# Kernel optimization log

Measured on AMD Instinct MI355X. Metric: run time of the kernel, lower is better.

The kernel has to match this reference:

```python
import jax, jax.numpy as jnp
import numpy as np

MU_F, SIGMA_F, ALPHA = 0.0789, 0.0774, 1.0
THRESH = MU_F + ALPHA * SIGMA_F
B, H, W = 8, 768, 768


def _gabor_kernel_real(frequency, theta):
    # skimage.filters.gabor_kernel with bandwidth=1, n_stds=3; real part only
    sigma = (1.0 / np.pi * np.sqrt(np.log(2.0) / 2.0) * 3.0) / frequency  # ~5.622
    ct, st = np.cos(theta), np.sin(theta)
    x0 = int(np.ceil(max(abs(3 * sigma * ct), abs(3 * sigma * st), 1.0)))
    y0 = int(np.ceil(max(abs(3 * sigma * st), abs(3 * sigma * ct), 1.0)))
    y, x = np.mgrid[-y0:y0 + 1, -x0:x0 + 1]
    rotx = x * ct + y * st
    roty = -x * st + y * ct
    g = np.exp(-0.5 * (rotx ** 2 + roty ** 2) / sigma ** 2) / (2 * np.pi * sigma ** 2)
    return (g * np.cos(2 * np.pi * frequency * rotx)).astype(np.float32)


# pre-flip 180deg so cross-correlation == scipy.ndimage.convolve (true convolution)
GABOR = [jnp.asarray(np.ascontiguousarray(_gabor_kernel_real(0.1, np.radians(a))[::-1, ::-1]))
         for a in (45, 90, 135, 180)]

_SIG = 0.3 * ((101 - 1) * 0.5 - 1) + 0.8  # cv2 sigma for ksize=101 when sigma=0 -> 15.5
_xg = np.arange(101, dtype=np.float64) - 50.0
_g = np.exp(-_xg ** 2 / (2 * _SIG ** 2))
GAUSS = jnp.asarray((_g / _g.sum()).astype(np.float32))
SOBEL_X = jnp.asarray(np.array([[-1, 0, 1], [-2, 0, 2], [-1, 0, 1]], np.float32))
SOBEL_Y = SOBEL_X.T


def _corr2d(img, k, mode):
    # 'same' cross-correlation with chosen boundary mode
    kh, kw = k.shape
    p = jnp.pad(img, ((kh // 2, kh // 2), (kw // 2, kw // 2)), mode=mode)
    return jax.lax.conv_general_dilated(p[None, None], k[None, None], (1, 1), 'VALID')[0, 0]


def _maxfilt3(img):
    # scipy.ndimage.maximum_filter(size=3, mode='reflect') == jnp 'symmetric' pad
    p = jnp.pad(img, 1, mode='symmetric')
    return jax.lax.reduce_window(p, -jnp.inf, jax.lax.max, (3, 3), (1, 1), 'VALID')


def _flood(maskf, seedf):
    # region growing == union of 8-connected components of {grad>=T} containing a seed;
    # iterate masked 3x3 dilation to fixed point
    reach0 = maskf * seedf

    def body(s):
        r, _ = s
        dil = jax.lax.reduce_window(jnp.pad(r, 1), 0.0, jax.lax.max, (3, 3), (1, 1), 'VALID')
        new = jnp.maximum(r, dil * maskf)
        return new, jnp.any(new != r)

    r, _ = jax.lax.while_loop(lambda s: s[1], body, (reach0, jnp.array(True)))
    return r


def _forward_one(pred, img):
    img = (img - img.min()) / (img.max() - img.min())
    # cv2.GaussianBlur((101,101), 0) with BORDER_REFLECT_101 -> 'reflect', separable
    bg = _corr2d(_corr2d(img, GAUSS[None, :], 'reflect'), GAUSS[:, None], 'reflect')
    enh = jnp.clip(img - bg, 0.0, 1.0)
    # seed points: Gabor line detection at 4 angles, local maxima above mean
    seed = jnp.zeros(enh.shape, bool)
    for k in GABOR:
        f = _corr2d(enh, k, 'symmetric')  # ndimage.convolve mode='reflect'
        seed = seed | ((f == _maxfilt3(f)) & (f > f.mean()))
    # Sobel gradient magnitude (cv2 default BORDER_REFLECT_101 -> 'reflect')
    gx = _corr2d(enh, SOBEL_X, 'reflect')
    gy = _corr2d(enh, SOBEL_Y, 'reflect')
    grad = jnp.sqrt(gx ** 2 + gy ** 2)
    maskf = (grad >= THRESH).astype(jnp.float32)
    seg = jax.lax.stop_gradient(_flood(maskf, seed.astype(jnp.float32)))
    # sigmoid only if prediction is outside [0,1]
    need_sig = (pred.max() > 1.0) | (pred.min() < 0.0)
    p = jnp.where(need_sig, jax.nn.sigmoid(pred), pred)
    return ((p > 0.5) | (seg > 0)).astype(jnp.float32)


def setup_inputs() -> dict:
    key = jax.random.key(0)
    k1, k2 = jax.random.split(key)
    unet_output = jax.random.normal(k1, (B, 1, H, W), jnp.float32) * 2.0  # logits
    original_image = jax.random.uniform(k2, (B, 1, H, W), jnp.float32)
    return {"unet_output": unet_output, "original_image": original_image}


def reference(unet_output, original_image):
    out = jax.vmap(_forward_one)(unet_output[:, 0], original_image[:, 0])
    return out[:, None]  # [B,1,H,W]
```

## Files before the change

kernel.cpp:

```cpp
#include <hip/hip_runtime.h>
#include <math.h>

typedef unsigned long long u64;

#define W 768
#define H 768
#define NP (768*768)
#define NB 8
#define WPR 12
#define NW (NB*H*WPR)
#define TH 16
#define P12N 73728
#define FLOOD_PASSES 6

#define PADI(q) ((q) + ((q) >> 5))


__device__ __forceinline__ unsigned fenc(float f) {
    unsigned b = __float_as_uint(f);
    return b ^ ((unsigned)((int)b >> 31) | 0x80000000u);
}
__device__ __forceinline__ float fdec(unsigned u) {
    unsigned b = (u & 0x80000000u) ? (u ^ 0x80000000u) : ~u;
    return __uint_as_float(b);
}
__device__ __forceinline__ int refl101(int i, int n) {
    if (i < 0) i = -i;
    if (i >= n) i = 2*n - 2 - i;
    return i;
}
__device__ __forceinline__ int symref(int i, int n) {
    if (i < 0) i = -1 - i;
    if (i >= n) i = 2*n - 1 - i;
    return i;
}

__global__ void initK(float* wtab, unsigned* sc) {
    int t = threadIdx.x;
    double sig = 15.5, ssum = 0.0;
    for (int i = 0; i < 101; i++) { double xx = i - 50; ssum += exp(-xx*xx/(2.0*sig*sig)); }
    for (int i = t; i < 107; i += 256) {
        float v = 0.f; int j = i - 3;
        if (j >= 0 && j < 101) { double xx = j - 50; v = (float)(exp(-xx*xx/(2.0*sig*sig))/ssum); }
        wtab[i] = v;
    }
    for (int i = t; i < 163; i += 256) {
        float v = 0.f; int j = i - 31;
        if (j >= 0 && j < 101) { double xx = j - 50; v = (float)(exp(-xx*xx/(2.0*sig*sig))/ssum); }
        wtab[128 + i] = v;
    }
    const double thetas[4] = {45.0, 90.0, 135.0, 180.0};
    const int    rad[4]    = {12, 17, 12, 17};
    const double sg = ((1.0/M_PI) * sqrt(log(2.0)/2.0) * 3.0) / 0.1;
    const double C  = 1.0/(2.0*M_PI*sg*sg);
    const int hG[6]   = {0, 0, 1, 2, 2, 3};
    const int hSin[6] = {0, 1, 0, 0, 1, 0};
    for (int idx = t; idx < 6*64; idx += 256) {
        int p = idx / 64, i = idx % 64;
        int g = hG[p], r = rad[g];
        double th = thetas[g] * (M_PI / 180.0);
        double a  = 2.0*M_PI*0.1*cos(th);
        float v = 0.f;
        int d = i - 20;
        if (i < 41 && d >= -r && d <= r) {
            double dd = (double)d, G = exp(-0.5*dd*dd/(sg*sg));
            v = hSin[p] ? (float)(C*G*sin(a*dd)) : (float)(C*G*cos(a*dd));
        }
        wtab[384 + p*64 + i] = v;
    }
    const int vG[6]   = {0, 0, 1, 2, 2, 3};
    const int vSin[6] = {0, 1, 0, 0, 1, 0};
    for (int idx = t; idx < 6*128; idx += 256) {
        int q = idx / 128, i = idx % 128;
        int g = vG[q], r = rad[g];
        double th = thetas[g] * (M_PI / 180.0);
        double bb = 2.0*M_PI*0.1*sin(th);
        float v = 0.f;
        int j = i - 31;
        if (j >= 0 && j <= 2*r) {
            double dd = (double)(j - r), G = exp(-0.5*dd*dd/(sg*sg));
            v = vSin[q] ? (float)(G*sin(bb*dd)) : (float)(G*cos(bb*dd));
        }
        wtab[768 + q*128 + i] = v;
    }
    if (t < 8)  { sc[t] = 0xFFFFFFFFu; sc[8+t] = 0u; sc[16+t] = 0xFFFFFFFFu; sc[24+t] = 0u; }
    if (t >= 32 && t < 64) ((float*)sc)[t] = 0.f;
    if (t >= 64 && t < 128) sc[t] = 0u;
}

__global__ void reduceK(const float* __restrict__ img, const float* __restrict__ pred,
                        unsigned* sc) {
    int b = blockIdx.y;
    int base = b*NP + blockIdx.x*9216 + threadIdx.x;
    float imn = INFINITY, imx = -INFINITY, pmn = INFINITY, pmx = -INFINITY;
    for (int k = 0; k < 36; k++) {
        float v = img[base + k*256];  imn = fminf(imn, v); imx = fmaxf(imx, v);
        float p = pred[base + k*256]; pmn = fminf(pmn, p); pmx = fmaxf(pmx, p);
    }
    for (int off = 32; off; off >>= 1) {
        imn = fminf(imn, __shfl_down(imn, off));
        imx = fmaxf(imx, __shfl_down(imx, off));
        pmn = fminf(pmn, __shfl_down(pmn, off));
        pmx = fmaxf(pmx, __shfl_down(pmx, off));
    }
    __shared__ float s[4][4];
    int lane = threadIdx.x & 63, wv = threadIdx.x >> 6;
    if (lane == 0) { s[0][wv] = imn; s[1][wv] = imx; s[2][wv] = pmn; s[3][wv] = pmx; }
    __syncthreads();
    if (threadIdx.x == 0) {
        float a0 = s[0][0], a1 = s[1][0], a2 = s[2][0], a3 = s[3][0];
        for (int w = 1; w < 4; w++) {
            a0 = fminf(a0, s[0][w]); a1 = fmaxf(a1, s[1][w]);
            a2 = fminf(a2, s[2][w]); a3 = fmaxf(a3, s[3][w]);
        }
        atomicMin(&sc[b],      fenc(a0));
        atomicMax(&sc[8 + b],  fenc(a1));
        atomicMin(&sc[16 + b], fenc(a2));
        atomicMax(&sc[24 + b], fenc(a3));
    }
}

__global__ __launch_bounds__(192) void gaussHK2(const float* __restrict__ img,
                                                float* __restrict__ out,
                                                const float* __restrict__ wt,
                                                const unsigned* __restrict__ sc) {
    int b = blockIdx.y, y = blockIdx.x, t = threadIdx.x;
    float mn = fdec(sc[b]), mx = fdec(sc[8 + b]);
    float den = mx - mn;
    __shared__ float sh[896];
    const float* row = img + ((size_t)b*H + y)*W;
    for (int q = t; q < 868; q += 192) {
        int gx = refl101(q - 50, W);
        sh[PADI(q)] = (row[gx] - mn) / den;
    }
    __syncthreads();
    float a0 = 0.f, a1 = 0.f, a2 = 0.f, a3 = 0.f;
    int qb = 4*t;
    #pragma unroll
    for (int p = 0; p < 104; p++) {
        float v = sh[PADI(qb + p)];
        a0 = __fmaf_rn(wt[p + 3], v, a0);
        a1 = __fmaf_rn(wt[p + 2], v, a1);
        a2 = __fmaf_rn(wt[p + 1], v, a2);
        a3 = __fmaf_rn(wt[p    ], v, a3);
    }
    float4 o; o.x = a0; o.y = a1; o.z = a2; o.w = a3;
    *(float4*)(out + ((size_t)b*H + y)*W + qb) = o;
}

__global__ __launch_bounds__(128) void gaussVK4(const float* __restrict__ tmp,
                                                const float* __restrict__ img,
                                                float* __restrict__ enh,
                                                const float* __restrict__ wt,
                                                const unsigned* __restrict__ sc) {
    int bid = blockIdx.x;
    int b = bid & 7; int r_ = bid >> 3; int tile = r_ % 48; int strip = r_ / 48;
    int y0 = tile*TH, x = strip*128 + threadIdx.x;
    float acc[TH];
    #pragma unroll
    for (int k = 0; k < TH; k++) acc[k] = 0.f;
    const float* T = tmp + (size_t)b*NP;
    for (int base = 0; base < 116; base += 4) {
        int g0 = refl101(y0+base-50, H), g1 = refl101(y0+base-49, H),
            g2 = refl101(y0+base-48, H), g3 = refl101(y0+base-47, H);
        float v0 = T[g0*W+x], v1 = T[g1*W+x], v2 = T[g2*W+x], v3 = T[g3*W+x];
        #pragma unroll
        for (int k = 0; k < TH; k++) {
            float a = acc[k];
            a = __fmaf_rn(wt[base   -k+31], v0, a);
            a = __fmaf_rn(wt[base+1 -k+31], v1, a);
            a = __fmaf_rn(wt[base+2 -k+31], v2, a);
            a = __fmaf_rn(wt[base+3 -k+31], v3, a);
            acc[k] = a;
        }
    }
    float mn = fdec(sc[b]), mx = fdec(sc[8 + b]);
    float den = mx - mn;
    #pragma unroll
    for (int k = 0; k < TH; k++) {
        size_t o = ((size_t)b*H + y0 + k)*W + x;
        float vv = (img[o] - mn) / den;
        float e = vv - acc[k];
        e = fminf(fmaxf(e, 0.f), 1.f);
        enh[o] = e;
    }
}

__global__ __launch_bounds__(192) void gaborHF4(const float* __restrict__ enh,
        float* __restrict__ h0c, float* __restrict__ h0s,
        float* __restrict__ h1c, float* __restrict__ h3c,
        const float* __restrict__ wt) {
    int b = blockIdx.y, y = blockIdx.x, t = threadIdx.x;
    __shared__ float sh[832];
    const float* row = enh + ((size_t)b*H + y)*W;
    for (int q = t; q < 802; q += 192) {
        int gx = symref(q - 17, W);
        sh[PADI(q)] = row[gx];
    }
    __syncthreads();
    const float* T0c = wt + 384; const float* T0s = wt + 448;
    const float* T1c = wt + 512; const float* T3c = wt + 704;
    float a0c[4] = {0,0,0,0}, a0s[4] = {0,0,0,0};
    float a1c[4] = {0,0,0,0}, a3c[4] = {0,0,0,0};
    int qb = 4*t;
    #pragma unroll
    for (int p = 0; p < 38; p++) {
        float v = sh[PADI(qb + p)];
        #pragma unroll
        for (int sub = 0; sub < 4; sub++) {
            int idx = p + 3 - sub;
            a0c[sub] = __fmaf_rn(T0c[idx], v, a0c[sub]);
            a0s[sub] = __fmaf_rn(T0s[idx], v, a0s[sub]);
            a1c[sub] = __fmaf_rn(T1c[idx], v, a1c[sub]);
            a3c[sub] = __fmaf_rn(T3c[idx], v, a3c[sub]);
        }
    }
    size_t o = ((size_t)b*H + y)*W + qb;
    *(float4*)(h0c + o) = make_float4(a0c[0], a0c[1], a0c[2], a0c[3]);
    *(float4*)(h0s + o) = make_float4(a0s[0], a0s[1], a0s[2], a0s[3]);
    *(float4*)(h1c + o) = make_float4(a1c[0], a1c[1], a1c[2], a1c[3]);
    *(float4*)(h3c + o) = make_float4(a3c[0], a3c[1], a3c[2], a3c[3]);
}

__global__ __launch_bounds__(128) void gaborVAB(
        const float* __restrict__ hc, const float* __restrict__ hs,
        float* __restrict__ f0, float* __restrict__ f2,
        const float* __restrict__ Tc, const float* __restrict__ Ts,
        float* __restrict__ p0, float* __restrict__ p2) {
    int bid = blockIdx.x;
    int b = bid & 7; int r_ = bid >> 3; int tile = r_ % 48; int strip = r_ / 48;
    int y0 = tile*TH, x = strip*128 + threadIdx.x;
    float A[TH], Bm[TH];
    #pragma unroll
    for (int k = 0; k < TH; k++) { A[k] = 0.f; Bm[k] = 0.f; }
    const size_t pb = (size_t)b*NP;
    for (int base = 0; base < 50; base += 2) {
        int gA = symref(y0 + base - 17, H), gB = symref(y0 + base - 16, H);
        size_t oA = pb + (size_t)gA*W + x, oB = pb + (size_t)gB*W + x;
        float vcA = hc[oA], vsA = hs[oA];
        float vcB = hc[oB], vsB = hs[oB];
        #pragma unroll
        for (int k = 0; k < TH; k++) {
            int i26 = base - k + 26;
            float t = A[k];
            t = __fmaf_rn(Tc[i26],   vcA, t);
            t = __fmaf_rn(Tc[i26+1], vcB, t);
            A[k] = t;
            t = Bm[k];
            t = __fmaf_rn(Ts[i26],   vsA, t);
            t = __fmaf_rn(Ts[i26+1], vsB, t);
            Bm[k] = t;
        }
    }
    int g64 = strip*2 + (threadIdx.x >> 6);
    bool l0 = (threadIdx.x & 63) == 0;
    #pragma unroll
    for (int k = 0; k < TH; k++) {
        size_t o = ((size_t)b*H + y0 + k)*W + x;
        size_t po = ((size_t)b*H + y0 + k)*12 + g64;
        float v0 = A[k] - Bm[k];
        float v2 = A[k] + Bm[k];
        f0[o] = v0;
        float s = v0;
        for (int off = 32; off; off >>= 1) s += __shfl_down(s, off);
        if (l0) p0[po] = s;
        f2[o] = v2;
        s = v2;
        for (int off = 32; off; off >>= 1) s += __shfl_down(s, off);
        if (l0) p2[po] = s;
    }
}

__global__ __launch_bounds__(128) void gaborV13(
        const float* __restrict__ h1, const float* __restrict__ h3,
        float* __restrict__ f1, float* __restrict__ f3,
        const float* __restrict__ T1, const float* __restrict__ T3,
        float* __restrict__ p1, float* __restrict__ p3) {
    int bid = blockIdx.x;
    int b = bid & 7; int r_ = bid >> 3; int tile = r_ % 48; int strip = r_ / 48;
    int y0 = tile*TH, x = strip*128 + threadIdx.x;
    float a1[TH], a3[TH];
    #pragma unroll
    for (int k = 0; k < TH; k++) { a1[k] = 0.f; a3[k] = 0.f; }
    const size_t pb = (size_t)b*NP;
    for (int base = 0; base < 50; base += 2) {
        int gA = symref(y0 + base - 17, H), gB = symref(y0 + base - 16, H);
        size_t oA = pb + (size_t)gA*W + x, oB = pb + (size_t)gB*W + x;
        float v1A = h1[oA], v3A = h3[oA];
        float v1B = h1[oB], v3B = h3[oB];
        #pragma unroll
        for (int k = 0; k < TH; k++) {
            int i31 = base - k + 31;
            float t = a1[k];
            t = __fmaf_rn(T1[i31],   v1A, t);
            t = __fmaf_rn(T1[i31+1], v1B, t);
            a1[k] = t;
            t = a3[k];
            t = __fmaf_rn(T3[i31],   v3A, t);
            t = __fmaf_rn(T3[i31+1], v3B, t);
            a3[k] = t;
        }
    }
    int g64 = strip*2 + (threadIdx.x >> 6);
    bool l0 = (threadIdx.x & 63) == 0;
    #pragma unroll
    for (int k = 0; k < TH; k++) {
        size_t o = ((size_t)b*H + y0 + k)*W + x;
        size_t po = ((size_t)b*H + y0 + k)*12 + g64;
        f1[o] = a1[k];
        float s = a1[k];
        for (int off = 32; off; off >>= 1) s += __shfl_down(s, off);
        if (l0) p1[po] = s;
        f3[o] = a3[k];
        s = a3[k];
        for (int off = 32; off; off >>= 1) s += __shfl_down(s, off);
        if (l0) p3[po] = s;
    }
}

__global__ void sumKAll(const float* __restrict__ p12, float* fsum) {
    int b = blockIdx.x, g = blockIdx.y, t = threadIdx.x;
    const float* P = p12 + (size_t)g*P12N;
    float s = 0.f;
    for (int k = 0; k < 9; k++) {
        int idx = t + k*256;
        int row = idx / 3, strip = idx - row*3;
        const float* Q = P + ((size_t)b*H + row)*12 + strip*4;
        float p4 = ((Q[0] + Q[1]) + Q[2]) + Q[3];
        s += p4;
    }
    __shared__ float sm[256];
    sm[t] = s; __syncthreads();
    for (int off = 128; off; off >>= 1) {
        if (t < off) sm[t] += sm[t + off];
        __syncthreads();
    }
    if (t == 0) fsum[g*8 + b] = sm[0];
}

__global__ __launch_bounds__(256) void seedK4(const float* __restrict__ f0,
        const float* __restrict__ f1, const float* __restrict__ f2,
        const float* __restrict__ f3, const float* __restrict__ fsum,
        u64* __restrict__ seedB) {
    int bid = blockIdx.x;
    int b = bid & 7; int r_ = bid >> 3;
    int y0 = (r_ % 48)*16; int xb = r_ / 48;
    int x0 = xb*256, t = threadIdx.x;
    __shared__ float sh[18][258];
    const float* planes[4] = {f0, f1, f2, f3};
    unsigned condMask = 0;
    #pragma unroll
    for (int a = 0; a < 4; a++) {
        const float* F = planes[a] + (size_t)b*NP;
        __syncthreads();
        for (int idx = t; idx < 18*258; idx += 256) {
            int rr = idx / 258, q = idx - rr*258;
            int gy = y0 - 1 + rr; gy = gy < 0 ? 0 : (gy > H-1 ? H-1 : gy);
            int gx = x0 - 1 + q;  gx = gx < 0 ? 0 : (gx > W-1 ? W-1 : gx);
            sh[rr][q] = F[gy*W + gx];
        }
        __syncthreads();
        float mean = fsum[a*8 + b] / 589824.f;
        #pragma unroll
        for (int r = 0; r < 16; r++) {
            float c = sh[r+1][t+1];
            float mx = c;
            mx = fmaxf(mx, sh[r  ][t]); mx = fmaxf(mx, sh[r  ][t+1]); mx = fmaxf(mx, sh[r  ][t+2]);
            mx = fmaxf(mx, sh[r+1][t]); mx = fmaxf(mx, sh[r+1][t+1]); mx = fmaxf(mx, sh[r+1][t+2]);
            mx = fmaxf(mx, sh[r+2][t]); mx = fmaxf(mx, sh[r+2][t+1]); mx = fmaxf(mx, sh[r+2][t+2]);
            if ((c == mx) && (c > mean)) condMask |= (1u << r);
        }
    }
    int wv = t >> 6, lane = t & 63;
    #pragma unroll
    for (int r = 0; r < 16; r++) {
        u64 m = __ballot((condMask >> r) & 1u);
        if (lane == 0)
            seedB[((size_t)b*H + y0 + r)*WPR + xb*4 + wv] = m;
    }
}

__global__ void sobelK(const float* __restrict__ enh, u64* __restrict__ maskB) {
    int bid = blockIdx.x;
    int b = bid & 7; int r_ = bid >> 3;
    int y = r_ / 3; int xs = r_ - 3*y;
    int x = xs*256 + threadIdx.x;
    const float* E = enh + (size_t)b*NP;
    int ym = y > 0 ? y-1 : 1, yp = y < H-1 ? y+1 : H-2;
    int xm = x > 0 ? x-1 : 1, xp = x < W-1 ? x+1 : W-2;
    float a00 = E[ym*W + xm], a01 = E[ym*W + x], a02 = E[ym*W + xp];
    float a10 = E[y*W + xm],                     a12 = E[y*W + xp];
    float a20 = E[yp*W + xm], a21 = E[yp*W + x], a22 = E[yp*W + xp];
    float gx = __fmaf_rn(-1.f, a00, 0.f);
    gx = __fmaf_rn( 1.f, a02, gx);
    gx = __fmaf_rn(-2.f, a10, gx);
    gx = __fmaf_rn( 2.f, a12, gx);
    gx = __fmaf_rn(-1.f, a20, gx);
    gx = __fmaf_rn( 1.f, a22, gx);
    float gy = __fmaf_rn(-1.f, a00, 0.f);
    gy = __fmaf_rn(-2.f, a01, gy);
    gy = __fmaf_rn(-1.f, a02, gy);
    gy = __fmaf_rn( 1.f, a20, gy);
    gy = __fmaf_rn( 2.f, a21, gy);
    gy = __fmaf_rn( 1.f, a22, gy);
    float s = __fadd_rn(__fmul_rn(gx, gx), __fmul_rn(gy, gy));
    float grad = (float)sqrt((double)s);
    const float THR = (float)(0.0789 + 1.0*0.0774);
    bool m = grad >= THR;
    u64 bits = __ballot(m);
    if ((threadIdx.x & 63) == 0) {
        int word = xs*4 + (threadIdx.x >> 6);
        maskB[((size_t)b*H + y)*WPR + word] = bits;
    }
}

__global__ __launch_bounds__(256) void floodTileK(const u64* __restrict__ Mb,
        const u64* __restrict__ seedB, u64* __restrict__ Rb,
        unsigned* __restrict__ chg, int t) {
    if (t > 0 && chg[t-1] == 0) return;
    int b = blockIdx.y;
    int y0 = blockIdx.x * 256;
    int ty = threadIdx.x;
    int y = y0 + ty;
    const u64* M = Mb + (size_t)b*H*WPR;
    const u64* S = seedB + (size_t)b*H*WPR;
    u64* R = Rb + (size_t)b*H*WPR;
    u64 m[12], r[12], hT[12], hB[12];
    #pragma unroll
    for (int w = 0; w < 12; w++) {
        m[w] = M[y*WPR + w];
        r[w] = (t == 0) ? (m[w] & S[y*WPR + w]) : R[y*WPR + w];
    }
    bool topRow = (ty == 0), botRow = (ty == 255);
    #pragma unroll
    for (int w = 0; w < 12; w++) { hT[w] = 0ULL; hB[w] = 0ULL; }
    if (topRow && y0 > 0) {
        int hy = y0 - 1;
        #pragma unroll
        for (int w = 0; w < 12; w++)
            hT[w] = (t == 0) ? (M[hy*WPR+w] & S[hy*WPR+w]) : R[hy*WPR+w];
    }
    if (botRow && y0 + 256 < H) {
        int hy = y0 + 256;
        #pragma unroll
        for (int w = 0; w < 12; w++)
            hB[w] = (t == 0) ? (M[hy*WPR+w] & S[hy*WPR+w]) : R[hy*WPR+w];
    }
    __shared__ u64 L[256][12];
    __shared__ unsigned chgArr[4];
    #pragma unroll
    for (int w = 0; w < 12; w++) L[ty][w] = r[w];
    __syncthreads();
    int wvid = ty >> 6, lane = ty & 63;
    bool grew = false;
    while (true) {
        u64 D[12], F[12];
        #pragma unroll
        for (int w = 0; w < 12; w++) {
            u64 up = topRow ? hT[w] : L[ty-1][w];
            u64 dn = botRow ? hB[w] : L[ty+1][w];
            D[w] = r[w] | up | dn;
        }
        #pragma unroll
        for (int w = 0; w < 12; w++) {
            u64 s = D[w] | (D[w] << 1) | (D[w] >> 1);
            if (w > 0)  s |= D[w-1] >> 63;
            if (w < 11) s |= D[w+1] << 63;
            F[w] = s & m[w];
        }
        {
            u64 c = 0;
            #pragma unroll
            for (int w = 0; w < 12; w++) {
                u64 sd = (F[w] | c) & m[w];
                u64 uf = m[w] & ~(m[w] + sd);
                F[w] = uf | sd;
                c = uf >> 63;
            }
        }
        {
            u64 c = 0;
            #pragma unroll
            for (int w = 11; w >= 0; w--) {
                u64 sd = (F[w] | (c << 63)) & m[w];
                u64 bm = __brevll(m[w]);
                u64 df = __brevll(bm & ~(bm + __brevll(sd)));
                F[w] = df | sd;
                c = df & 1ULL;
            }
        }
        bool chgT = false;
        #pragma unroll
        for (int w = 0; w < 12; w++) if (F[w] != r[w]) chgT = true;
        bool wc = __any(chgT);
        if (lane == 0) chgArr[wvid] = wc ? 1u : 0u;
        __syncthreads();
        #pragma unroll
        for (int w = 0; w < 12; w++) { r[w] = F[w]; L[ty][w] = F[w]; }
        unsigned any = chgArr[0] | chgArr[1] | chgArr[2] | chgArr[3];
        __syncthreads();
        if (!any) break;
        grew = true;
    }
    #pragma unroll
    for (int w = 0; w < 12; w++) R[y*WPR + w] = r[w];
    if (grew && ty == 0) atomicOr(&chg[t], 1u);
}

__global__ void finalK(const float* __restrict__ pred, const u64* __restrict__ reachB,
                       const unsigned* __restrict__ sc, float* __restrict__ out) {
    int b = blockIdx.z, y = blockIdx.y, x = blockIdx.x*256 + threadIdx.x;
    float pmn = fdec(sc[16 + b]), pmx = fdec(sc[24 + b]);
    bool needSig = (pmx > 1.0f) || (pmn < 0.0f);
    float p = pred[((size_t)b*H + y)*W + x];
    float pv;
    if (needSig) {
        float e = (float)exp(-(double)p);
        pv = 1.f / (1.f + e);
    } else {
        pv = p;
    }
    bool on = pv > 0.5f;
    u64 w = reachB[((size_t)b*H + y)*WPR + (x >> 6)];
    on = on || ((w >> (x & 63)) & 1ULL);
    out[((size_t)b*H + y)*W + x] = on ? 1.f : 0.f;
}

extern "C" void kernel_launch(void* const* d_in, const int* in_sizes, int n_in,
                              void* d_out, int out_size, void* d_ws, size_t ws_size,
                              hipStream_t stream) {
    const float* pred = (const float*)d_in[0];
    const float* img  = (const float*)d_in[1];
    float* out = (float*)d_out;
    char* ws = (char*)d_ws;

    float*    wtab   = (float*)(ws + 1024);
    unsigned* sc     = (unsigned*)(ws + 16384);
    float*    fsum   = ((float*)sc) + 32;
    unsigned* chg    = sc + 64;
    float*    p12    = (float*)(ws + 20480);
    u64*      maskB  = (u64*)(ws + 1310720);
    u64*      seedB  = (u64*)(ws + 1900544);
    u64*      reachB = (u64*)(ws + 2490368);
    const size_t PL = (size_t)NB*NP;
    float* plane = (float*)(ws + 4194304);
    float* b0  = plane;
    float* b1  = plane + PL;
    float* h0c = plane + 2*PL; float* h0s = plane + 3*PL;
    float* h1c = plane + 4*PL; float* h3c = plane + 5*PL;
    float* f0  = plane + 8*PL; float* f1 = plane + 9*PL;
    float* f2  = plane + 10*PL; float* f3 = plane + 11*PL;

    const float* gpadH = wtab;
    const float* gpadV = wtab + 128;

    initK<<<1, 256, 0, stream>>>(wtab, sc);
    reduceK<<<dim3(64, 8), 256, 0, stream>>>(img, pred, sc);

    dim3 gRow(768, 8);
    gaussHK2<<<gRow, 192, 0, stream>>>(img, b0, gpadH, sc);
    gaussVK4<<<2304, 128, 0, stream>>>(b0, img, b1, gpadV, sc);

    sobelK<<<18432, 256, 0, stream>>>(b1, maskB);

    gaborHF4<<<gRow, 192, 0, stream>>>(b1, h0c, h0s, h1c, h3c, wtab);

    gaborVAB<<<2304, 128, 0, stream>>>(h0c, h0s, f0, f2,
                                       wtab + 768, wtab + 896,
                                       p12, p12 + 2*P12N);
    gaborV13<<<2304, 128, 0, stream>>>(h1c, h3c, f1, f3,
                                       wtab + 1024, wtab + 1408,
                                       p12 + P12N, p12 + 3*P12N);
    sumKAll<<<dim3(8, 4), 256, 0, stream>>>(p12, fsum);

    seedK4<<<1152, 256, 0, stream>>>(f0, f1, f2, f3, fsum, seedB);

    for (int t = 0; t < FLOOD_PASSES; t++)
        floodTileK<<<dim3(3, 8), 256, 0, stream>>>(maskB, seedB, reachB, chg, t);

    finalK<<<dim3(3, H, 8), 256, 0, stream>>>(pred, reachB, sc, out);
}
```

Measured before the change: 254.8 us.

## Fuse seed detection into vertical Gabor passes and compute filter means analytically

The vertical Gabor kernels now compute the 3x3 local-max seed test in registers, using shuffles and shared memory for neighbours, and write seed bitmasks directly. This removes the four full-resolution filter-response planes and the separate seed kernel. Tile-boundary columns are spilled to a small buffer and finished by a tiny edge kernel. Each filter's global mean is now computed from row sums of the enhanced image using precomputed boundary-aware weight tables, instead of reducing the responses. The cost is recomputing two halo rows per tile and added code complexity.

```diff
diff --git a/kernel.cpp b/kernel.cpp
--- a/kernel.cpp
+++ b/kernel.cpp
@@ -10,7 +10,6 @@
 #define WPR 12
 #define NW (NB*H*WPR)
 #define TH 16
-#define P12N 73728
 #define FLOOD_PASSES 6
 
 #define PADI(q) ((q) + ((q) >> 5))
@@ -34,8 +33,11 @@
     if (i >= n) i = 2*n - 1 - i;
     return i;
 }
-
-__global__ void initK(float* wtab, unsigned* sc) {
+__device__ __forceinline__ size_t fbIdx(int g, int b, int strip, int c4, int row) {
+    return ((((size_t)g*NB + b)*6 + strip)*4 + c4)*768 + row;
+}
+
+__global__ void initK(float* wtab, float* cwv, unsigned* sc) {
     int t = threadIdx.x;
     double sig = 15.5, ssum = 0.0;
     for (int i = 0; i < 101; i++) { double xx = i - 50; ssum += exp(-xx*xx/(2.0*sig*sig)); }
@@ -86,6 +88,42 @@
     if (t < 8)  { sc[t] = 0xFFFFFFFFu; sc[8+t] = 0u; sc[16+t] = 0xFFFFFFFFu; sc[24+t] = 0u; }
     if (t >= 32 && t < 64) ((float*)sc)[t] = 0.f;
     if (t >= 64 && t < 128) sc[t] = 0u;
+    __syncthreads();
+    const int hTab[4] = {0, 1, 2, 5};
+    const int vTab[4] = {0, 1, 2, 5};
+    const int Rv[4]   = {12, 12, 17, 17};
+    if (t < 4) {
+        const float* T = wtab + 384 + hTab[t]*64;
+        float s = 0.f;
+        for (int i = 0; i < 41; i++) s += T[i];
+        wtab[1808 + t] = s;
+    }
+    for (int idx = t; idx < 4*68; idx += 256) {
+        int ch = idx / 68, e = idx % 68;
+        int c = (e < 34) ? e : 734 + (e - 34);
+        const float* T = wtab + 384 + hTab[ch]*64;
+        float w = 0.f;
+        int lo = c - 767; if (lo < -20) lo = -20;
+        int hi = c;       if (hi > 20)  hi = 20;
+        for (int d = lo; d <= hi; d++) w += T[d + 20];
+        if (c <= 19)  { for (int d = -20; d <= -1 - c; d++) w += T[d + 20]; }
+        if (c >= 748) { for (int d = 768 - c; d <= 20; d++) w += T[d + 20]; }
+        float s = 0.f;
+        for (int i = 0; i < 41; i++) s += T[i];
+        wtab[1536 + ch*68 + e] = w - s;
+    }
+    for (int idx = t; idx < 4*768; idx += 256) {
+        int ch = idx / 768, r = idx % 768;
+        const float* V = wtab + 768 + vTab[ch]*128;
+        int off = 31 + Rv[ch];
+        float w = 0.f;
+        int lo = r - 767; if (lo < -17) lo = -17;
+        int hi = r;       if (hi > 17)  hi = 17;
+        for (int e = lo; e <= hi; e++) w += V[off + e];
+        if (r <= 16)  { for (int e = -17; e <= -1 - r; e++) w += V[off + e]; }
+        if (r >= 751) { for (int e = 768 - r; e <= 17; e++) w += V[off + e]; }
+        cwv[ch*768 + r] = w;
+    }
 }
 
 __global__ void reduceK(const float* __restrict__ img, const float* __restrict__ pred,
@@ -152,7 +190,8 @@
                                                 const float* __restrict__ img,
                                                 float* __restrict__ enh,
                                                 const float* __restrict__ wt,
-                                                const unsigned* __restrict__ sc) {
+                                                const unsigned* __restrict__ sc,
+                                                float* __restrict__ rsP) {
     int bid = blockIdx.x;
     int b = bid & 7; int r_ = bid >> 3; int tile = r_ % 48; int strip = r_ / 48;
     int y0 = tile*TH, x = strip*128 + threadIdx.x;
@@ -176,6 +215,8 @@
     }
     float mn = fdec(sc[b]), mx = fdec(sc[8 + b]);
     float den = mx - mn;
+    int g64 = strip*2 + (threadIdx.x >> 6);
+    bool l0 = (threadIdx.x & 63) == 0;
     #pragma unroll
     for (int k = 0; k < TH; k++) {
         size_t o = ((size_t)b*H + y0 + k)*W + x;
@@ -183,6 +224,48 @@
         float e = vv - acc[k];
         e = fminf(fmaxf(e, 0.f), 1.f);
         enh[o] = e;
+        float s = e;
+        for (int off = 32; off; off >>= 1) s += __shfl_down(s, off);
+        if (l0) rsP[((size_t)b*H + y0 + k)*12 + g64] = s;
+    }
+}
+
+__global__ __launch_bounds__(256) void meanK(const float* __restrict__ rsP,
+        const float* __restrict__ enh, const float* __restrict__ wtab,
+        const float* __restrict__ cwv, float* __restrict__ fsum) {
+    int b = blockIdx.x, t = threadIdx.x;
+    float S[4] = {0.f, 0.f, 0.f, 0.f};
+    for (int rr = 0; rr < 3; rr++) {
+        int r = t + rr*256;
+        const float* P = rsP + ((size_t)b*H + r)*12;
+        float rs = 0.f;
+        for (int j = 0; j < 12; j++) rs += P[j];
+        const float* E = enh + (size_t)b*NP + (size_t)r*W;
+        #pragma unroll
+        for (int ch = 0; ch < 4; ch++) {
+            float RS = wtab[1808 + ch] * rs;
+            const float* dw = wtab + 1536 + ch*68;
+            for (int e = 0; e < 34; e++)  RS = __fmaf_rn(dw[e], E[e], RS);
+            for (int e = 34; e < 68; e++) RS = __fmaf_rn(dw[e], E[700 + e], RS);
+            S[ch] = __fmaf_rn(cwv[ch*768 + r], RS, S[ch]);
+        }
+    }
+    __shared__ float sm[256];
+    __shared__ float chres[4];
+    for (int ch = 0; ch < 4; ch++) {
+        sm[t] = S[ch]; __syncthreads();
+        for (int off = 128; off; off >>= 1) {
+            if (t < off) sm[t] += sm[t + off];
+            __syncthreads();
+        }
+        if (t == 0) chres[ch] = sm[0];
+        __syncthreads();
+    }
+    if (t == 0) {
+        fsum[0*8 + b] = chres[0] - chres[1];
+        fsum[1*8 + b] = chres[2];
+        fsum[2*8 + b] = chres[0] + chres[1];
+        fsum[3*8 + b] = chres[3];
     }
 }
 
@@ -222,161 +305,276 @@
     *(float4*)(h3c + o) = make_float4(a3c[0], a3c[1], a3c[2], a3c[3]);
 }
 
-__global__ __launch_bounds__(128) void gaborVAB(
+__global__ __launch_bounds__(128) void gaborVAB2(
         const float* __restrict__ hc, const float* __restrict__ hs,
-        float* __restrict__ f0, float* __restrict__ f2,
         const float* __restrict__ Tc, const float* __restrict__ Ts,
-        float* __restrict__ p0, float* __restrict__ p2) {
+        const float* __restrict__ fsum, u64* __restrict__ seedAB,
+        float* __restrict__ fb) {
     int bid = blockIdx.x;
     int b = bid & 7; int r_ = bid >> 3; int tile = r_ % 48; int strip = r_ / 48;
     int y0 = tile*TH, x = strip*128 + threadIdx.x;
-    float A[TH], Bm[TH];
-    #pragma unroll
-    for (int k = 0; k < TH; k++) { A[k] = 0.f; Bm[k] = 0.f; }
+    float A[18], B[18];
+    #pragma unroll
+    for (int k = 0; k < 18; k++) { A[k] = 0.f; B[k] = 0.f; }
     const size_t pb = (size_t)b*NP;
-    for (int base = 0; base < 50; base += 2) {
-        int gA = symref(y0 + base - 17, H), gB = symref(y0 + base - 16, H);
+    for (int bb = 0; bb < 52; bb += 2) {
+        int gA = symref(y0 + bb - 18, H), gB = symref(y0 + bb - 17, H);
         size_t oA = pb + (size_t)gA*W + x, oB = pb + (size_t)gB*W + x;
         float vcA = hc[oA], vsA = hs[oA];
         float vcB = hc[oB], vsB = hs[oB];
         #pragma unroll
-        for (int k = 0; k < TH; k++) {
-            int i26 = base - k + 26;
-            float t = A[k];
+        for (int kk = 0; kk < 18; kk++) {
+            int i26 = bb - kk + 26;
+            float t = A[kk];
             t = __fmaf_rn(Tc[i26],   vcA, t);
             t = __fmaf_rn(Tc[i26+1], vcB, t);
-            A[k] = t;
-            t = Bm[k];
+            A[kk] = t;
+            t = B[kk];
             t = __fmaf_rn(Ts[i26],   vsA, t);
             t = __fmaf_rn(Ts[i26+1], vsB, t);
-            Bm[k] = t;
-        }
-    }
-    int g64 = strip*2 + (threadIdx.x >> 6);
-    bool l0 = (threadIdx.x & 63) == 0;
-    #pragma unroll
-    for (int k = 0; k < TH; k++) {
-        size_t o = ((size_t)b*H + y0 + k)*W + x;
-        size_t po = ((size_t)b*H + y0 + k)*12 + g64;
-        float v0 = A[k] - Bm[k];
-        float v2 = A[k] + Bm[k];
-        f0[o] = v0;
-        float s = v0;
-        for (int off = 32; off; off >>= 1) s += __shfl_down(s, off);
-        if (l0) p0[po] = s;
-        f2[o] = v2;
-        s = v2;
-        for (int off = 32; off; off >>= 1) s += __shfl_down(s, off);
-        if (l0) p2[po] = s;
-    }
-}
-
-__global__ __launch_bounds__(128) void gaborV13(
+            B[kk] = t;
+        }
+    }
+    if (tile == 0)  { A[0] = A[1];   B[0] = B[1]; }
+    if (tile == 47) { A[17] = A[16]; B[17] = B[16]; }
+
+    int lane = threadIdx.x & 63, wv = threadIdx.x >> 6;
+    bool edgeLane = (wv == 0 && lane == 0) || (wv == 1 && lane == 63);
+    float mean0 = fsum[0*8 + b] / 589824.f;
+    float mean2 = fsum[2*8 + b] / 589824.f;
+    __shared__ float vmEdge[2][16];
+    unsigned cond = 0;
+    {
+        float vm[16], c[16];
+        float fm = A[0] - B[0], f0 = A[1] - B[1];
+        #pragma unroll
+        for (int k = 0; k < 16; k++) {
+            float fp = A[k+2] - B[k+2];
+            vm[k] = fmaxf(fmaxf(fm, f0), fp);
+            c[k] = f0;
+            fm = f0; f0 = fp;
+        }
+        if (wv == 0 && lane == 63) {
+            #pragma unroll
+            for (int k = 0; k < 16; k++) vmEdge[0][k] = vm[k];
+        }
+        if (wv == 1 && lane == 0)  {
+            #pragma unroll
+            for (int k = 0; k < 16; k++) vmEdge[1][k] = vm[k];
+        }
+        __syncthreads();
+        #pragma unroll
+        for (int k = 0; k < 16; k++) {
+            float vl = __shfl_up(vm[k], 1);
+            float vr = __shfl_down(vm[k], 1);
+            if (wv == 1 && lane == 0)  vl = vmEdge[0][k];
+            if (wv == 0 && lane == 63) vr = vmEdge[1][k];
+            float mx = fmaxf(fmaxf(vl, vm[k]), vr);
+            if ((c[k] == mx) && (c[k] > mean0) && !edgeLane) cond |= 1u << k;
+        }
+        __syncthreads();
+    }
+    {
+        float vm[16], c[16];
+        float fm = A[0] + B[0], f0 = A[1] + B[1];
+        #pragma unroll
+        for (int k = 0; k < 16; k++) {
+            float fp = A[k+2] + B[k+2];
+            vm[k] = fmaxf(fmaxf(fm, f0), fp);
+            c[k] = f0;
+            fm = f0; f0 = fp;
+        }
+        if (wv == 0 && lane == 63) {
+            #pragma unroll
+            for (int k = 0; k < 16; k++) vmEdge[0][k] = vm[k];
+        }
+        if (wv == 1 && lane == 0)  {
+            #pragma unroll
+            for (int k = 0; k < 16; k++) vmEdge[1][k] = vm[k];
+        }
+        __syncthreads();
+        #pragma unroll
+        for (int k = 0; k < 16; k++) {
+            float vl = __shfl_up(vm[k], 1);
+            float vr = __shfl_down(vm[k], 1);
+            if (wv == 1 && lane == 0)  vl = vmEdge[0][k];
+            if (wv == 0 && lane == 63) vr = vmEdge[1][k];
+            float mx = fmaxf(fmaxf(vl, vm[k]), vr);
+            if ((c[k] == mx) && (c[k] > mean2) && !edgeLane) cond |= 1u << k;
+        }
+    }
+    #pragma unroll
+    for (int k = 0; k < 16; k++) {
+        u64 bits = __ballot((cond >> k) & 1u);
+        if (lane == 0)
+            seedAB[((size_t)b*H + y0 + k)*WPR + strip*2 + wv] = bits;
+    }
+    int c4 = -1;
+    if (wv == 0 && lane == 0) c4 = 0;
+    else if (wv == 0 && lane == 1) c4 = 1;
+    else if (wv == 1 && lane == 62) c4 = 2;
+    else if (wv == 1 && lane == 63) c4 = 3;
+    if (c4 >= 0) {
+        for (int kk = 1; kk <= 16; kk++) {
+            int row = y0 + kk - 1;
+            fb[fbIdx(0, b, strip, c4, row)] = A[kk] - B[kk];
+            fb[fbIdx(2, b, strip, c4, row)] = A[kk] + B[kk];
+        }
+    }
+}
+
+__global__ __launch_bounds__(128) void gaborV13_2(
         const float* __restrict__ h1, const float* __restrict__ h3,
-        float* __restrict__ f1, float* __restrict__ f3,
         const float* __restrict__ T1, const float* __restrict__ T3,
-        float* __restrict__ p1, float* __restrict__ p3) {
+        const float* __restrict__ fsum, u64* __restrict__ seed13,
+        float* __restrict__ fb) {
     int bid = blockIdx.x;
     int b = bid & 7; int r_ = bid >> 3; int tile = r_ % 48; int strip = r_ / 48;
     int y0 = tile*TH, x = strip*128 + threadIdx.x;
-    float a1[TH], a3[TH];
-    #pragma unroll
-    for (int k = 0; k < TH; k++) { a1[k] = 0.f; a3[k] = 0.f; }
+    float A1[18], A3[18];
+    #pragma unroll
+    for (int k = 0; k < 18; k++) { A1[k] = 0.f; A3[k] = 0.f; }
     const size_t pb = (size_t)b*NP;
-    for (int base = 0; base < 50; base += 2) {
-        int gA = symref(y0 + base - 17, H), gB = symref(y0 + base - 16, H);
+    for (int bb = 0; bb < 52; bb += 2) {
+        int gA = symref(y0 + bb - 18, H), gB = symref(y0 + bb - 17, H);
         size_t oA = pb + (size_t)gA*W + x, oB = pb + (size_t)gB*W + x;
         float v1A = h1[oA], v3A = h3[oA];
         float v1B = h1[oB], v3B = h3[oB];
         #pragma unroll
-        for (int k = 0; k < TH; k++) {
-            int i31 = base - k + 31;
-            float t = a1[k];
+        for (int kk = 0; kk < 18; kk++) {
+            int i31 = bb - kk + 31;
+            float t = A1[kk];
             t = __fmaf_rn(T1[i31],   v1A, t);
             t = __fmaf_rn(T1[i31+1], v1B, t);
-            a1[k] = t;
-            t = a3[k];
+            A1[kk] = t;
+            t = A3[kk];
             t = __fmaf_rn(T3[i31],   v3A, t);
             t = __fmaf_rn(T3[i31+1], v3B, t);
-            a3[k] = t;
-        }
-    }
-    int g64 = strip*2 + (threadIdx.x >> 6);
-    bool l0 = (threadIdx.x & 63) == 0;
-    #pragma unroll
-    for (int k = 0; k < TH; k++) {
-        size_t o = ((size_t)b*H + y0 + k)*W + x;
-        size_t po = ((size_t)b*H + y0 + k)*12 + g64;
-        f1[o] = a1[k];
-        float s = a1[k];
-        for (int off = 32; off; off >>= 1) s += __shfl_down(s, off);
-        if (l0) p1[po] = s;
-        f3[o] = a3[k];
-        s = a3[k];
-        for (int off = 32; off; off >>= 1) s += __shfl_down(s, off);
-        if (l0) p3[po] = s;
-    }
-}
-
-__global__ void sumKAll(const float* __restrict__ p12, float* fsum) {
-    int b = blockIdx.x, g = blockIdx.y, t = threadIdx.x;
-    const float* P = p12 + (size_t)g*P12N;
-    float s = 0.f;
-    for (int k = 0; k < 9; k++) {
-        int idx = t + k*256;
-        int row = idx / 3, strip = idx - row*3;
-        const float* Q = P + ((size_t)b*H + row)*12 + strip*4;
-        float p4 = ((Q[0] + Q[1]) + Q[2]) + Q[3];
-        s += p4;
-    }
-    __shared__ float sm[256];
-    sm[t] = s; __syncthreads();
-    for (int off = 128; off; off >>= 1) {
-        if (t < off) sm[t] += sm[t + off];
-        __syncthreads();
-    }
-    if (t == 0) fsum[g*8 + b] = sm[0];
-}
-
-__global__ __launch_bounds__(256) void seedK4(const float* __restrict__ f0,
-        const float* __restrict__ f1, const float* __restrict__ f2,
-        const float* __restrict__ f3, const float* __restrict__ fsum,
-        u64* __restrict__ seedB) {
-    int bid = blockIdx.x;
-    int b = bid & 7; int r_ = bid >> 3;
-    int y0 = (r_ % 48)*16; int xb = r_ / 48;
-    int x0 = xb*256, t = threadIdx.x;
-    __shared__ float sh[18][258];
-    const float* planes[4] = {f0, f1, f2, f3};
-    unsigned condMask = 0;
-    #pragma unroll
-    for (int a = 0; a < 4; a++) {
-        const float* F = planes[a] + (size_t)b*NP;
-        __syncthreads();
-        for (int idx = t; idx < 18*258; idx += 256) {
-            int rr = idx / 258, q = idx - rr*258;
-            int gy = y0 - 1 + rr; gy = gy < 0 ? 0 : (gy > H-1 ? H-1 : gy);
-            int gx = x0 - 1 + q;  gx = gx < 0 ? 0 : (gx > W-1 ? W-1 : gx);
-            sh[rr][q] = F[gy*W + gx];
-        }
-        __syncthreads();
-        float mean = fsum[a*8 + b] / 589824.f;
-        #pragma unroll
-        for (int r = 0; r < 16; r++) {
-            float c = sh[r+1][t+1];
-            float mx = c;
-            mx = fmaxf(mx, sh[r  ][t]); mx = fmaxf(mx, sh[r  ][t+1]); mx = fmaxf(mx, sh[r  ][t+2]);
-            mx = fmaxf(mx, sh[r+1][t]); mx = fmaxf(mx, sh[r+1][t+1]); mx = fmaxf(mx, sh[r+1][t+2]);
-            mx = fmaxf(mx, sh[r+2][t]); mx = fmaxf(mx, sh[r+2][t+1]); mx = fmaxf(mx, sh[r+2][t+2]);
-            if ((c == mx) && (c > mean)) condMask |= (1u << r);
-        }
-    }
-    int wv = t >> 6, lane = t & 63;
-    #pragma unroll
-    for (int r = 0; r < 16; r++) {
-        u64 m = __ballot((condMask >> r) & 1u);
+            A3[kk] = t;
+        }
+    }
+    if (tile == 0)  { A1[0] = A1[1];   A3[0] = A3[1]; }
+    if (tile == 47) { A1[17] = A1[16]; A3[17] = A3[16]; }
+
+    int lane = threadIdx.x & 63, wv = threadIdx.x >> 6;
+    bool edgeLane = (wv == 0 && lane == 0) || (wv == 1 && lane == 63);
+    float mean1 = fsum[1*8 + b] / 589824.f;
+    float mean3 = fsum[3*8 + b] / 589824.f;
+    __shared__ float vmEdge[2][16];
+    unsigned cond = 0;
+    {
+        float vm[16], c[16];
+        float fm = A1[0], f0 = A1[1];
+        #pragma unroll
+        for (int k = 0; k < 16; k++) {
+            float fp = A1[k+2];
+            vm[k] = fmaxf(fmaxf(fm, f0), fp);
+            c[k] = f0;
+            fm = f0; f0 = fp;
+        }
+        if (wv == 0 && lane == 63) {
+            #pragma unroll
+            for (int k = 0; k < 16; k++) vmEdge[0][k] = vm[k];
+        }
+        if (wv == 1 && lane == 0)  {
+            #pragma unroll
+            for (int k = 0; k < 16; k++) vmEdge[1][k] = vm[k];
+        }
+        __syncthreads();
+        #pragma unroll
+        for (int k = 0; k < 16; k++) {
+            float vl = __shfl_up(vm[k], 1);
+            float vr = __shfl_down(vm[k], 1);
+            if (wv == 1 && lane == 0)  vl = vmEdge[0][k];
+            if (wv == 0 && lane == 63) vr = vmEdge[1][k];
+            float mx = fmaxf(fmaxf(vl, vm[k]), vr);
+            if ((c[k] == mx) && (c[k] > mean1) && !edgeLane) cond |= 1u << k;
+        }
+        __syncthreads();
+    }
+    {
+        float vm[16], c[16];
+        float fm = A3[0], f0 = A3[1];
+        #pragma unroll
+        for (int k = 0; k < 16; k++) {
+            float fp = A3[k+2];
+            vm[k] = fmaxf(fmaxf(fm, f0), fp);
+            c[k] = f0;
+            fm = f0; f0 = fp;
+        }
+        if (wv == 0 && lane == 63) {
+            #pragma unroll
+            for (int k = 0; k < 16; k++) vmEdge[0][k] = vm[k];
+        }
+        if (wv == 1 && lane == 0)  {
+            #pragma unroll
+            for (int k = 0; k < 16; k++) vmEdge[1][k] = vm[k];
+        }
+        __syncthreads();
+        #pragma unroll
+        for (int k = 0; k < 16; k++) {
+            float vl = __shfl_up(vm[k], 1);
+            float vr = __shfl_down(vm[k], 1);
+            if (wv == 1 && lane == 0)  vl = vmEdge[0][k];
+            if (wv == 0 && lane == 63) vr = vmEdge[1][k];
+            float mx = fmaxf(fmaxf(vl, vm[k]), vr);
+            if ((c[k] == mx) && (c[k] > mean3) && !edgeLane) cond |= 1u << k;
+        }
+    }
+    #pragma unroll
+    for (int k = 0; k < 16; k++) {
+        u64 bits = __ballot((cond >> k) & 1u);
         if (lane == 0)
-            seedB[((size_t)b*H + y0 + r)*WPR + xb*4 + wv] = m;
+            seed13[((size_t)b*H + y0 + k)*WPR + strip*2 + wv] = bits;
+    }
+    int c4 = -1;
+    if (wv == 0 && lane == 0) c4 = 0;
+    else if (wv == 0 && lane == 1) c4 = 1;
+    else if (wv == 1 && lane == 62) c4 = 2;
+    else if (wv == 1 && lane == 63) c4 = 3;
+    if (c4 >= 0) {
+        for (int kk = 1; kk <= 16; kk++) {
+            int row = y0 + kk - 1;
+            fb[fbIdx(1, b, strip, c4, row)] = A1[kk];
+            fb[fbIdx(3, b, strip, c4, row)] = A3[kk];
+        }
+    }
+}
+
+__global__ __launch_bounds__(768) void seedEdgeK(const float* __restrict__ fb,
+        const float* __restrict__ fsum, u64* __restrict__ seedAB) {
+    int b = blockIdx.x, r = threadIdx.x;
+    float mean[4];
+    #pragma unroll
+    for (int g = 0; g < 4; g++) mean[g] = fsum[g*8 + b] / 589824.f;
+    int rm = r > 0 ? r - 1 : 0, rp = r < 767 ? r + 1 : 767;
+    for (int s = 0; s < 6; s++) {
+        for (int side = 0; side < 2; side++) {
+            bool any = false;
+            #pragma unroll
+            for (int g = 0; g < 4; g++) {
+                const float *pm1, *p0, *pp1;
+                if (side == 0) {
+                    pm1 = fb + fbIdx(g, b, (s == 0) ? 0 : s - 1, (s == 0) ? 0 : 3, 0);
+                    p0  = fb + fbIdx(g, b, s, 0, 0);
+                    pp1 = fb + fbIdx(g, b, s, 1, 0);
+                } else {
+                    pm1 = fb + fbIdx(g, b, s, 2, 0);
+                    p0  = fb + fbIdx(g, b, s, 3, 0);
+                    pp1 = fb + fbIdx(g, b, (s == 5) ? 5 : s + 1, (s == 5) ? 3 : 0, 0);
+                }
+                float c = p0[r];
+                float mx = c;
+                mx = fmaxf(mx, pm1[rm]); mx = fmaxf(mx, pm1[r]); mx = fmaxf(mx, pm1[rp]);
+                mx = fmaxf(mx, p0[rm]);  mx = fmaxf(mx, p0[rp]);
+                mx = fmaxf(mx, pp1[rm]); mx = fmaxf(mx, pp1[r]); mx = fmaxf(mx, pp1[rp]);
+                any = any || ((c == mx) && (c > mean[g]));
+            }
+            if (any) {
+                size_t o = ((size_t)b*H + r)*WPR + s*2 + side;
+                seedAB[o] |= side ? (1ULL << 63) : 1ULL;
+            }
+        }
     }
 }
 
@@ -415,21 +613,22 @@
 }
 
 __global__ __launch_bounds__(256) void floodTileK(const u64* __restrict__ Mb,
-        const u64* __restrict__ seedB, u64* __restrict__ Rb,
-        unsigned* __restrict__ chg, int t) {
+        const u64* __restrict__ S1, const u64* __restrict__ S2,
+        u64* __restrict__ Rb, unsigned* __restrict__ chg, int t) {
     if (t > 0 && chg[t-1] == 0) return;
     int b = blockIdx.y;
     int y0 = blockIdx.x * 256;
     int ty = threadIdx.x;
     int y = y0 + ty;
     const u64* M = Mb + (size_t)b*H*WPR;
-    const u64* S = seedB + (size_t)b*H*WPR;
+    const u64* SA = S1 + (size_t)b*H*WPR;
+    const u64* SB = S2 + (size_t)b*H*WPR;
     u64* R = Rb + (size_t)b*H*WPR;
     u64 m[12], r[12], hT[12], hB[12];
     #pragma unroll
     for (int w = 0; w < 12; w++) {
         m[w] = M[y*WPR + w];
-        r[w] = (t == 0) ? (m[w] & S[y*WPR + w]) : R[y*WPR + w];
+        r[w] = (t == 0) ? (m[w] & (SA[y*WPR + w] | SB[y*WPR + w])) : R[y*WPR + w];
     }
     bool topRow = (ty == 0), botRow = (ty == 255);
     #pragma unroll
@@ -438,13 +637,13 @@
         int hy = y0 - 1;
         #pragma unroll
         for (int w = 0; w < 12; w++)
-            hT[w] = (t == 0) ? (M[hy*WPR+w] & S[hy*WPR+w]) : R[hy*WPR+w];
+            hT[w] = (t == 0) ? (M[hy*WPR+w] & (SA[hy*WPR+w] | SB[hy*WPR+w])) : R[hy*WPR+w];
     }
     if (botRow && y0 + 256 < H) {
         int hy = y0 + 256;
         #pragma unroll
         for (int w = 0; w < 12; w++)
-            hB[w] = (t == 0) ? (M[hy*WPR+w] & S[hy*WPR+w]) : R[hy*WPR+w];
+            hB[w] = (t == 0) ? (M[hy*WPR+w] & (SA[hy*WPR+w] | SB[hy*WPR+w])) : R[hy*WPR+w];
     }
     __shared__ u64 L[256][12];
     __shared__ unsigned chgArr[4];
@@ -535,48 +734,46 @@
     char* ws = (char*)d_ws;
 
     float*    wtab   = (float*)(ws + 1024);
-    unsigned* sc     = (unsigned*)(ws + 16384);
+    float*    cwv    = (float*)(ws + 12288);
+    unsigned* sc     = (unsigned*)(ws + 24576);
     float*    fsum   = ((float*)sc) + 32;
     unsigned* chg    = sc + 64;
-    float*    p12    = (float*)(ws + 20480);
-    u64*      maskB  = (u64*)(ws + 1310720);
-    u64*      seedB  = (u64*)(ws + 1900544);
-    u64*      reachB = (u64*)(ws + 2490368);
+    float*    rsP    = (float*)(ws + 28672);
+    float*    fb     = (float*)(ws + 327680);
+    u64*      maskB  = (u64*)(ws + 2752512);
+    u64*      seedAB = (u64*)(ws + 3407872);
+    u64*      seed13 = (u64*)(ws + 4063232);
+    u64*      reachB = (u64*)(ws + 4718592);
     const size_t PL = (size_t)NB*NP;
-    float* plane = (float*)(ws + 4194304);
+    float* plane = (float*)(ws + 8388608);
     float* b0  = plane;
     float* b1  = plane + PL;
     float* h0c = plane + 2*PL; float* h0s = plane + 3*PL;
     float* h1c = plane + 4*PL; float* h3c = plane + 5*PL;
-    float* f0  = plane + 8*PL; float* f1 = plane + 9*PL;
-    float* f2  = plane + 10*PL; float* f3 = plane + 11*PL;
 
     const float* gpadH = wtab;
     const float* gpadV = wtab + 128;
 
-    initK<<<1, 256, 0, stream>>>(wtab, sc);
+    initK<<<1, 256, 0, stream>>>(wtab, cwv, sc);
     reduceK<<<dim3(64, 8), 256, 0, stream>>>(img, pred, sc);
 
     dim3 gRow(768, 8);
     gaussHK2<<<gRow, 192, 0, stream>>>(img, b0, gpadH, sc);
-    gaussVK4<<<2304, 128, 0, stream>>>(b0, img, b1, gpadV, sc);
-
+    gaussVK4<<<2304, 128, 0, stream>>>(b0, img, b1, gpadV, sc, rsP);
+
+    meanK<<<8, 256, 0, stream>>>(rsP, b1, wtab, cwv, fsum);
     sobelK<<<18432, 256, 0, stream>>>(b1, maskB);
 
     gaborHF4<<<gRow, 192, 0, stream>>>(b1, h0c, h0s, h1c, h3c, wtab);
 
-    gaborVAB<<<2304, 128, 0, stream>>>(h0c, h0s, f0, f2,
-                                       wtab + 768, wtab + 896,
-                                       p12, p12 + 2*P12N);
-    gaborV13<<<2304, 128, 0, stream>>>(h1c, h3c, f1, f3,
-                                       wtab + 1024, wtab + 1408,
-                                       p12 + P12N, p12 + 3*P12N);
-    sumKAll<<<dim3(8, 4), 256, 0, stream>>>(p12, fsum);
-
-    seedK4<<<1152, 256, 0, stream>>>(f0, f1, f2, f3, fsum, seedB);
+    gaborVAB2<<<2304, 128, 0, stream>>>(h0c, h0s, wtab + 768, wtab + 896,
+                                        fsum, seedAB, fb);
+    gaborV13_2<<<2304, 128, 0, stream>>>(h1c, h3c, wtab + 1024, wtab + 1408,
+                                         fsum, seed13, fb);
+    seedEdgeK<<<8, 768, 0, stream>>>(fb, fsum, seedAB);
 
     for (int t = 0; t < FLOOD_PASSES; t++)
-        floodTileK<<<dim3(3, 8), 256, 0, stream>>>(maskB, seedB, reachB, chg, t);
+        floodTileK<<<dim3(3, 8), 256, 0, stream>>>(maskB, seedAB, seed13, reachB, chg, t);
 
     finalK<<<dim3(3, H, 8), 256, 0, stream>>>(pred, reachB, sc, out);
 }
```

Result: slower. 332.0 us (+30.3%).
